# Kernel optimization log

Measured on AMD Instinct MI355X. Metric: run time of the kernel, lower is better.

The kernel has to match this reference:

```python
import jax, jax.numpy as jnp
import numpy as np

B, D, H, S = 65536, 256, 4, 64
HD = D // H  # head_dim = 64
EPS = 1e-8


def _lin(x, W, b):
    # torch nn.Linear: y = x @ W.T + b, W: [out, in]
    return x @ W.T + b


def _cos_attn(q_heads, keys, vals):
    # q_heads: [B,H,hd]; keys/vals: [H,S,hd] (shared across batch)
    qn = q_heads / (jnp.linalg.norm(q_heads, axis=-1, keepdims=True) + EPS)
    kn = keys / (jnp.linalg.norm(keys, axis=-1, keepdims=True) + EPS)
    sim = jnp.einsum('bhd,hsd->bhs', qn, kn)          # cosine sims, temp=1.0
    attn = jax.nn.softmax(sim, axis=-1)
    return jnp.einsum('bhs,hsd->bhd', attn, vals)     # [B,H,hd]


def setup_inputs() -> dict:
    key = jax.random.key(0)
    ks = jax.random.split(key, 20)

    def xavier(k, shape):
        fan_in, fan_out = shape[1], shape[0]
        lim = np.sqrt(6.0 / (fan_in + fan_out))
        return jax.random.uniform(k, shape, jnp.float32, -lim, lim)

    return {
        'query': jax.random.normal(ks[0], (B, D), jnp.float32),
        'context': jax.random.normal(ks[1], (B, D), jnp.float32),
        'fast_keys': 0.01 * jax.random.normal(ks[2], (H, S, HD), jnp.float32),
        'fast_vals': 0.01 * jax.random.normal(ks[3], (H, S, HD), jnp.float32),
        'deep_keys': 0.01 * jax.random.normal(ks[4], (H, S, HD), jnp.float32),
        'deep_vals': 0.01 * jax.random.normal(ks[5], (H, S, HD), jnp.float32),
        'Wq': xavier(ks[6], (D, D)), 'bq': jnp.zeros((D,), jnp.float32),
        'Wg': xavier(ks[7], (D, D)), 'bg': jnp.zeros((D,), jnp.float32),
        'Wc1': xavier(ks[8], (D // 2, D)), 'bc1': jnp.zeros((D // 2,), jnp.float32),
        'Wc2': xavier(ks[9], (1, D // 2)), 'bc2': jnp.zeros((1,), jnp.float32),
        'Wo': xavier(ks[10], (D, D)), 'bo': jnp.zeros((D,), jnp.float32),
        'Ws': xavier(ks[11], (D, D)), 'bs': jnp.zeros((D,), jnp.float32),
        'mix_logit': jnp.zeros((), jnp.float32),
        'surprise_mean': jnp.zeros((1, D), jnp.float32),
        'surprise_var': jnp.ones((1, D), jnp.float32),
    }


def reference(query, context, fast_keys, fast_vals, deep_keys, deep_vals,
              Wq, bq, Wg, bg, Wc1, bc1, Wc2, bc2, Wo, bo, Ws, bs,
              mix_logit, surprise_mean, surprise_var):
    # --- query projection and head split ---
    q = _lin(query, Wq, bq)                       # [B, D]
    q_heads = q.reshape(B, H, HD)                 # [B, H, hd]

    # --- dual-tier cosine-similarity attention reads ---
    v_fast = _cos_attn(q_heads, fast_keys, fast_vals).reshape(B, D)
    v_deep = _cos_attn(q_heads, deep_keys, deep_vals).reshape(B, D)

    # --- context-gated mixing of tiers ---
    gate = jnp.tanh(_lin(context, Wg, bg)).mean(axis=-1, keepdims=True)  # [B,1]
    mix = jax.nn.sigmoid(mix_logit + gate)
    out = mix * v_fast + (1.0 - mix) * v_deep

    # --- adaptive retrieval confidence head ---
    conf = jax.nn.sigmoid(_lin(jnp.tanh(_lin(context, Wc1, bc1)), Wc2, bc2))  # [B,1]
    out = out * conf
    out = _lin(out, Wo, bo)                       # [B, d_value]

    # --- surprise (detached diagnostic, does not feed output) ---
    h = jax.lax.stop_gradient(_lin(context, Ws, bs))
    z = (h - surprise_mean) / jnp.sqrt(surprise_var + 1e-6)
    surprise = jax.nn.sigmoid(jnp.abs(z).mean(axis=-1) - 2.0)  # 1/max(0.5,0.1)=2.0
    del surprise  # aux diagnostic; main output is the retrieved vector
    return out
```

## Files before the change

### kernel.cpp

```cpp
#include <hip/hip_runtime.h>

typedef unsigned short u16;
typedef __attribute__((ext_vector_type(8))) short bf16x8;
typedef __attribute__((ext_vector_type(4))) float f32x4;
typedef __attribute__((ext_vector_type(4))) unsigned short u16x4;

#define MFMA16(a, b, c) __builtin_amdgcn_mfma_f32_16x16x32_bf16((a), (b), (c), 0, 0, 0)

#define OFF_WQ   0
#define OFF_WG   65536
#define OFF_WC1  131072
#define OFF_WO   163840
#define OFF_KNF  229376
#define OFF_VTF  245760
#define OFF_KND  262144
#define OFF_VTD  278528

__device__ __forceinline__ u16 f2b(float f) {
  union { float f; unsigned u; } v; v.f = f;
  unsigned r = v.u + 0x7fffu + ((v.u >> 16) & 1u);
  return (u16)(r >> 16);
}
__device__ __forceinline__ float fsig(float x) {
  return __builtin_amdgcn_rcpf(1.f + __expf(-x));
}
__device__ __forceinline__ float ftanh(float x) {
  float e = __expf(2.f * x);
  return (e - 1.f) * __builtin_amdgcn_rcpf(e + 1.f);
}
__device__ __forceinline__ float sum16(float v) {
  v += __shfl_xor(v, 1);
  v += __shfl_xor(v, 2);
  v += __shfl_xor(v, 4);
  v += __shfl_xor(v, 8);
  return v;
}

__global__ void k_convert(const float* __restrict__ Wq, const float* __restrict__ Wg,
                          const float* __restrict__ Wc1, const float* __restrict__ Wo,
                          u16* __restrict__ ws) {
  int i = blockIdx.x * 256 + threadIdx.x;
  ws[OFF_WQ + i] = f2b(Wq[i]);
  ws[OFF_WG + i] = f2b(Wg[i]);
  ws[OFF_WO + i] = f2b(Wo[i]);
  if (i < 32768) ws[OFF_WC1 + i] = f2b(Wc1[i]);
}

__global__ void k_prep(const float* __restrict__ fk, const float* __restrict__ fv,
                       const float* __restrict__ dk, const float* __restrict__ dv,
                       u16* __restrict__ ws) {
  int t = blockIdx.x * 64 + threadIdx.x;
  int h = t >> 6, s = t & 63;
  const float* p;
  float ss, sc;

  p = fk + t * 64; ss = 0.f;
  for (int d = 0; d < 64; ++d) { float x = p[d]; ss += x * x; }
  sc = __builtin_amdgcn_rcpf(__builtin_amdgcn_sqrtf(ss) + 1e-8f);
  for (int d = 0; d < 64; ++d) ws[OFF_KNF + t * 64 + d] = f2b(p[d] * sc);

  p = dk + t * 64; ss = 0.f;
  for (int d = 0; d < 64; ++d) { float x = p[d]; ss += x * x; }
  sc = __builtin_amdgcn_rcpf(__builtin_amdgcn_sqrtf(ss) + 1e-8f);
  for (int d = 0; d < 64; ++d) ws[OFF_KND + t * 64 + d] = f2b(p[d] * sc);

  p = fv + t * 64;
  for (int d = 0; d < 64; ++d) ws[OFF_VTF + h * 4096 + d * 64 + s] = f2b(p[d]);
  p = dv + t * 64;
  for (int d = 0; d < 64; ++d) ws[OFF_VTD + h * 4096 + d * 64 + s] = f2b(p[d]);
}

__global__ __launch_bounds__(256, 2)
void k_fused(const float* __restrict__ query, const float* __restrict__ context,
             const float* __restrict__ bq, const float* __restrict__ bg,
             const float* __restrict__ bc1, const float* __restrict__ Wc2,
             const float* __restrict__ bc2v, const float* __restrict__ bo,
             const float* __restrict__ mixl, const u16* __restrict__ ws,
             float* __restrict__ outp) {
  __shared__ u16 sX[64 * 256];
  __shared__ float red_g[4][64];
  __shared__ float red_c[4][64];
  __shared__ float sA[64];
  __shared__ float sB[64];

  const int t = threadIdx.x;
  const int w = t >> 6;
  const int lane = t & 63;
  const int quad = lane >> 4;
  const int l16 = lane & 15;
  const int row4 = quad * 4;
  const int blk = blockIdx.x;
  char* Xb = (char*)sX;
  char* chunk = Xb + w * 8192;

  auto stage = [&](const float* src) {
    #pragma unroll
    for (int i = 0; i < 16; ++i) {
      int e = i * 1024 + t * 4;
      float4 v = *(const float4*)(src + e);
      int row = e >> 8, col = e & 255;
      u16x4 pk;
      pk.x = f2b(v.x); pk.y = f2b(v.y); pk.z = f2b(v.z); pk.w = f2b(v.w);
      *(u16x4*)(Xb + row * 512 + ((((col >> 3) ^ (row & 7)) << 4) | ((col & 7) << 1))) = pk;
    }
  };
  auto ldA = [&](int row, int kb) {
    return *(const bf16x8*)(Xb + row * 512 + ((((kb >> 3) ^ (row & 7)) << 4)));
  };
  auto ldC = [&](int row, int kb) {
    return *(const bf16x8*)(chunk + row * 128 + ((((kb >> 3) ^ (row & 7)) << 4)));
  };
  auto cwr = [&](int row, int col, u16 v) {
    *(u16*)(chunk + row * 128 + (((((col >> 3) ^ (row & 7)) << 3) | (col & 7)) << 1)) = v;
  };

  const f32x4 vzero = {0.f, 0.f, 0.f, 0.f};

  stage(context + (size_t)blk * 16384);
  __syncthreads();

  {
    f32x4 acc[4][4];
    #pragma unroll
    for (int mt = 0; mt < 4; ++mt)
      #pragma unroll
      for (int nt = 0; nt < 4; ++nt) acc[mt][nt] = vzero;
    const u16* WB = ws + OFF_WG + (w * 64 + l16) * 256;
    #pragma unroll
    for (int kk = 0; kk < 8; ++kk) {
      int kb = kk * 32 + quad * 8;
      bf16x8 a0 = ldA(l16, kb), a1 = ldA(16 + l16, kb), a2 = ldA(32 + l16, kb), a3 = ldA(48 + l16, kb);
      #pragma unroll
      for (int nt = 0; nt < 4; ++nt) {
        bf16x8 b = *(const bf16x8*)(WB + nt * 4096 + kb);
        acc[0][nt] = MFMA16(a0, b, acc[0][nt]);
        acc[1][nt] = MFMA16(a1, b, acc[1][nt]);
        acc[2][nt] = MFMA16(a2, b, acc[2][nt]);
        acc[3][nt] = MFMA16(a3, b, acc[3][nt]);
      }
    }
    float bgv[4];
    #pragma unroll
    for (int nt = 0; nt < 4; ++nt) bgv[nt] = bg[w * 64 + nt * 16 + l16];
    #pragma unroll
    for (int mt = 0; mt < 4; ++mt)
      #pragma unroll
      for (int r = 0; r < 4; ++r) {
        float s = 0.f;
        #pragma unroll
        for (int nt = 0; nt < 4; ++nt) s += ftanh(acc[mt][nt][r] + bgv[nt]);
        s = sum16(s);
        if (l16 == 0) red_g[w][mt * 16 + row4 + r] = s;
      }
  }
  {
    f32x4 acc[4][2];
    #pragma unroll
    for (int mt = 0; mt < 4; ++mt) { acc[mt][0] = vzero; acc[mt][1] = vzero; }
    const u16* WB = ws + OFF_WC1 + (w * 32 + l16) * 256;
    #pragma unroll
    for (int kk = 0; kk < 8; ++kk) {
      int kb = kk * 32 + quad * 8;
      bf16x8 a0 = ldA(l16, kb), a1 = ldA(16 + l16, kb), a2 = ldA(32 + l16, kb), a3 = ldA(48 + l16, kb);
      #pragma unroll
      for (int nt = 0; nt < 2; ++nt) {
        bf16x8 b = *(const bf16x8*)(WB + nt * 4096 + kb);
        acc[0][nt] = MFMA16(a0, b, acc[0][nt]);
        acc[1][nt] = MFMA16(a1, b, acc[1][nt]);
        acc[2][nt] = MFMA16(a2, b, acc[2][nt]);
        acc[3][nt] = MFMA16(a3, b, acc[3][nt]);
      }
    }
    float bcv[2], wcv[2];
    #pragma unroll
    for (int nt = 0; nt < 2; ++nt) {
      int n = w * 32 + nt * 16 + l16;
      bcv[nt] = bc1[n]; wcv[nt] = Wc2[n];
    }
    #pragma unroll
    for (int mt = 0; mt < 4; ++mt)
      #pragma unroll
      for (int r = 0; r < 4; ++r) {
        float s = 0.f;
        #pragma unroll
        for (int nt = 0; nt < 2; ++nt) s += ftanh(acc[mt][nt][r] + bcv[nt]) * wcv[nt];
        s = sum16(s);
        if (l16 == 0) red_c[w][mt * 16 + row4 + r] = s;
      }
  }
  __syncthreads();
  if (t < 64) {
    float g = (red_g[0][t] + red_g[1][t] + red_g[2][t] + red_g[3][t]) * (1.f / 256.f);
    float mix = fsig(mixl[0] + g);
    float conf = fsig(red_c[0][t] + red_c[1][t] + red_c[2][t] + red_c[3][t] + bc2v[0]);
    sA[t] = conf * mix;
    sB[t] = conf - conf * mix;
  }
  __syncthreads();

  stage(query + (size_t)blk * 16384);
  __syncthreads();

  f32x4 qa[4][4];
  {
    #pragma unroll
    for (int mt = 0; mt < 4; ++mt)
      #pragma unroll
      for (int nt = 0; nt < 4; ++nt) qa[mt][nt] = vzero;
    const u16* WB = ws + OFF_WQ + (w * 64 + l16) * 256;
    #pragma unroll
    for (int kk = 0; kk < 8; ++kk) {
      int kb = kk * 32 + quad * 8;
      bf16x8 a0 = ldA(l16, kb), a1 = ldA(16 + l16, kb), a2 = ldA(32 + l16, kb), a3 = ldA(48 + l16, kb);
      #pragma unroll
      for (int nt = 0; nt < 4; ++nt) {
        bf16x8 b = *(const bf16x8*)(WB + nt * 4096 + kb);
        qa[0][nt] = MFMA16(a0, b, qa[0][nt]);
        qa[1][nt] = MFMA16(a1, b, qa[1][nt]);
        qa[2][nt] = MFMA16(a2, b, qa[2][nt]);
        qa[3][nt] = MFMA16(a3, b, qa[3][nt]);
      }
    }
    float bqv[4];
    #pragma unroll
    for (int nt = 0; nt < 4; ++nt) bqv[nt] = bq[w * 64 + nt * 16 + l16];
    #pragma unroll
    for (int mt = 0; mt < 4; ++mt)
      #pragma unroll
      for (int nt = 0; nt < 4; ++nt)
        #pragma unroll
        for (int r = 0; r < 4; ++r) qa[mt][nt][r] += bqv[nt];
  }
  float scl[4][4];
  #pragma unroll
  for (int mt = 0; mt < 4; ++mt)
    #pragma unroll
    for (int r = 0; r < 4; ++r) {
      float ss = 0.f;
      #pragma unroll
      for (int nt = 0; nt < 4; ++nt) ss += qa[mt][nt][r] * qa[mt][nt][r];
      ss = sum16(ss);
      scl[mt][r] = __builtin_amdgcn_rcpf(__builtin_amdgcn_sqrtf(ss) + 1e-8f);
    }
  __syncthreads();

  #pragma unroll
  for (int mt = 0; mt < 4; ++mt)
    #pragma unroll
    for (int r = 0; r < 4; ++r) {
      int row = mt * 16 + row4 + r;
      #pragma unroll
      for (int nt = 0; nt < 4; ++nt)
        cwr(row, nt * 16 + l16, f2b(qa[mt][nt][r] * scl[mt][r]));
    }

  f32x4 sf[4][4], sd[4][4];
  #pragma unroll
  for (int mt = 0; mt < 4; ++mt)
    #pragma unroll
    for (int nt = 0; nt < 4; ++nt) { sf[mt][nt] = vzero; sd[mt][nt] = vzero; }
  {
    const u16* knF = ws + OFF_KNF + w * 4096;
    const u16* knD = ws + OFF_KND + w * 4096;
    #pragma unroll
    for (int kk = 0; kk < 2; ++kk) {
      int kb = kk * 32 + quad * 8;
      bf16x8 a0 = ldC(l16, kb), a1 = ldC(16 + l16, kb), a2 = ldC(32 + l16, kb), a3 = ldC(48 + l16, kb);
      #pragma unroll
      for (int nt = 0; nt < 4; ++nt) {
        bf16x8 bF = *(const bf16x8*)(knF + (nt * 16 + l16) * 64 + kb);
        bf16x8 bD = *(const bf16x8*)(knD + (nt * 16 + l16) * 64 + kb);
        sf[0][nt] = MFMA16(a0, bF, sf[0][nt]);
        sf[1][nt] = MFMA16(a1, bF, sf[1][nt]);
        sf[2][nt] = MFMA16(a2, bF, sf[2][nt]);
        sf[3][nt] = MFMA16(a3, bF, sf[3][nt]);
        sd[0][nt] = MFMA16(a0, bD, sd[0][nt]);
        sd[1][nt] = MFMA16(a1, bD, sd[1][nt]);
        sd[2][nt] = MFMA16(a2, bD, sd[2][nt]);
        sd[3][nt] = MFMA16(a3, bD, sd[3][nt]);
      }
    }
  }

  f32x4 oacc[4][4];
  {
    #pragma unroll
    for (int mt = 0; mt < 4; ++mt)
      #pragma unroll
      for (int r = 0; r < 4; ++r) {
        float rs = 0.f;
        #pragma unroll
        for (int nt = 0; nt < 4; ++nt) { float e = __expf(sf[mt][nt][r]); sf[mt][nt][r] = e; rs += e; }
        rs = sum16(rs);
        float inv = __builtin_amdgcn_rcpf(rs);
        int row = mt * 16 + row4 + r;
        #pragma unroll
        for (int nt = 0; nt < 4; ++nt) cwr(row, nt * 16 + l16, f2b(sf[mt][nt][r] * inv));
      }
    f32x4 pv[4][4];
    #pragma unroll
    for (int mt = 0; mt < 4; ++mt)
      #pragma unroll
      for (int nt = 0; nt < 4; ++nt) pv[mt][nt] = vzero;
    const u16* vT = ws + OFF_VTF + w * 4096;
    #pragma unroll
    for (int kk = 0; kk < 2; ++kk) {
      int kb = kk * 32 + quad * 8;
      bf16x8 a0 = ldC(l16, kb), a1 = ldC(16 + l16, kb), a2 = ldC(32 + l16, kb), a3 = ldC(48 + l16, kb);
      #pragma unroll
      for (int nt = 0; nt < 4; ++nt) {
        bf16x8 b = *(const bf16x8*)(vT + (nt * 16 + l16) * 64 + kb);
        pv[0][nt] = MFMA16(a0, b, pv[0][nt]);
        pv[1][nt] = MFMA16(a1, b, pv[1][nt]);
        pv[2][nt] = MFMA16(a2, b, pv[2][nt]);
        pv[3][nt] = MFMA16(a3, b, pv[3][nt]);
      }
    }
    #pragma unroll
    for (int mt = 0; mt < 4; ++mt)
      #pragma unroll
      for (int r = 0; r < 4; ++r) {
        float m_ = sA[mt * 16 + row4 + r];
        #pragma unroll
        for (int nt = 0; nt < 4; ++nt) oacc[mt][nt][r] = m_ * pv[mt][nt][r];
      }
  }
  {
    #pragma unroll
    for (int mt = 0; mt < 4; ++mt)
      #pragma unroll
      for (int r = 0; r < 4; ++r) {
        float rs = 0.f;
        #pragma unroll
        for (int nt = 0; nt < 4; ++nt) { float e = __expf(sd[mt][nt][r]); sd[mt][nt][r] = e; rs += e; }
        rs = sum16(rs);
        float inv = __builtin_amdgcn_rcpf(rs);
        int row = mt * 16 + row4 + r;
        #pragma unroll
        for (int nt = 0; nt < 4; ++nt) cwr(row, nt * 16 + l16, f2b(sd[mt][nt][r] * inv));
      }
    f32x4 pv[4][4];
    #pragma unroll
    for (int mt = 0; mt < 4; ++mt)
      #pragma unroll
      for (int nt = 0; nt < 4; ++nt) pv[mt][nt] = vzero;
    const u16* vT = ws + OFF_VTD + w * 4096;
    #pragma unroll
    for (int kk = 0; kk < 2; ++kk) {
      int kb = kk * 32 + quad * 8;
      bf16x8 a0 = ldC(l16, kb), a1 = ldC(16 + l16, kb), a2 = ldC(32 + l16, kb), a3 = ldC(48 + l16, kb);
      #pragma unroll
      for (int nt = 0; nt < 4; ++nt) {
        bf16x8 b = *(const bf16x8*)(vT + (nt * 16 + l16) * 64 + kb);
        pv[0][nt] = MFMA16(a0, b, pv[0][nt]);
        pv[1][nt] = MFMA16(a1, b, pv[1][nt]);
        pv[2][nt] = MFMA16(a2, b, pv[2][nt]);
        pv[3][nt] = MFMA16(a3, b, pv[3][nt]);
      }
    }
    #pragma unroll
    for (int mt = 0; mt < 4; ++mt)
      #pragma unroll
      for (int r = 0; r < 4; ++r) {
        float m_ = sB[mt * 16 + row4 + r];
        #pragma unroll
        for (int nt = 0; nt < 4; ++nt) oacc[mt][nt][r] += m_ * pv[mt][nt][r];
      }
  }

  __syncthreads();
  #pragma unroll
  for (int mt = 0; mt < 4; ++mt)
    #pragma unroll
    for (int r = 0; r < 4; ++r) {
      int row = mt * 16 + row4 + r;
      #pragma unroll
      for (int nt = 0; nt < 4; ++nt) {
        int col = w * 64 + nt * 16 + l16;
        *(u16*)(Xb + row * 512 + (((((col >> 3) ^ (row & 7)) << 3) | (col & 7)) << 1)) =
            f2b(oacc[mt][nt][r]);
      }
    }
  __syncthreads();

  {
    f32x4 o[4][4];
    #pragma unroll
    for (int mt = 0; mt < 4; ++mt)
      #pragma unroll
      for (int nt = 0; nt < 4; ++nt) o[mt][nt] = vzero;
    const u16* WB = ws + OFF_WO + (w * 64 + l16) * 256;
    #pragma unroll
    for (int kk = 0; kk < 8; ++kk) {
      int kb = kk * 32 + quad * 8;
      bf16x8 a0 = ldA(l16, kb), a1 = ldA(16 + l16, kb), a2 = ldA(32 + l16, kb), a3 = ldA(48 + l16, kb);
      #pragma unroll
      for (int nt = 0; nt < 4; ++nt) {
        bf16x8 b = *(const bf16x8*)(WB + nt * 4096 + kb);
        o[0][nt] = MFMA16(a0, b, o[0][nt]);
        o[1][nt] = MFMA16(a1, b, o[1][nt]);
        o[2][nt] = MFMA16(a2, b, o[2][nt]);
        o[3][nt] = MFMA16(a3, b, o[3][nt]);
      }
    }
    float bov[4];
    #pragma unroll
    for (int nt = 0; nt < 4; ++nt) bov[nt] = bo[w * 64 + nt * 16 + l16];
    float* dst = outp + (size_t)blk * 16384;
    #pragma unroll
    for (int mt = 0; mt < 4; ++mt)
      #pragma unroll
      for (int r = 0; r < 4; ++r) {
        int row = mt * 16 + row4 + r;
        #pragma unroll
        for (int nt = 0; nt < 4; ++nt)
          dst[row * 256 + w * 64 + nt * 16 + l16] = o[mt][nt][r] + bov[nt];
      }
  }
}

extern "C" void kernel_launch(void* const* d_in, const int* in_sizes, int n_in,
                              void* d_out, int out_size, void* d_ws, size_t ws_size,
                              hipStream_t stream) {
  const float* query   = (const float*)d_in[0];
  const float* context = (const float*)d_in[1];
  const float* fk      = (const float*)d_in[2];
  const float* fv      = (const float*)d_in[3];
  const float* dk      = (const float*)d_in[4];
  const float* dv      = (const float*)d_in[5];
  const float* Wq      = (const float*)d_in[6];
  const float* bq      = (const float*)d_in[7];
  const float* Wg      = (const float*)d_in[8];
  const float* bg      = (const float*)d_in[9];
  const float* Wc1     = (const float*)d_in[10];
  const float* bc1     = (const float*)d_in[11];
  const float* Wc2     = (const float*)d_in[12];
  const float* bc2     = (const float*)d_in[13];
  const float* Wo      = (const float*)d_in[14];
  const float* bo      = (const float*)d_in[15];
  const float* mixl    = (const float*)d_in[18];
  u16* ws = (u16*)d_ws;
  float* outp = (float*)d_out;

  k_convert<<<256, 256, 0, stream>>>(Wq, Wg, Wc1, Wo, ws);
  k_prep<<<4, 64, 0, stream>>>(fk, fv, dk, dv, ws);
  k_fused<<<1024, 256, 0, stream>>>(query, context, bq, bg, bc1, Wc2, bc2, bo,
                                    mixl, ws, outp);
}
```

Baseline: 323.9 us.

## Halve rows per block to raise occupancy and parallelize key prep per element

The fused kernel now processes 32 batch rows per block instead of 64, using twice as many blocks, half the shared memory and half the accumulator registers, with launch bounds raised to 4 blocks per CU. The key/value prep kernel is reworked from one thread per key row with serial loops into one block per key row, with a wave-wide shuffle reduction for the norm. This aims to improve latency hiding and remove the serial prep bottleneck. In exchange, each weight B-fragment loaded from global memory is reused across only two M-tiles instead of four, so weight traffic per row doubles.

```diff
diff --git a/kernel.cpp b/kernel.cpp
--- a/kernel.cpp
+++ b/kernel.cpp
@@ -35,6 +35,15 @@
   v += __shfl_xor(v, 8);
   return v;
 }
+__device__ __forceinline__ float sum64(float v) {
+  v += __shfl_xor(v, 1);
+  v += __shfl_xor(v, 2);
+  v += __shfl_xor(v, 4);
+  v += __shfl_xor(v, 8);
+  v += __shfl_xor(v, 16);
+  v += __shfl_xor(v, 32);
+  return v;
+}
 
 __global__ void k_convert(const float* __restrict__ Wq, const float* __restrict__ Wg,
                           const float* __restrict__ Wc1, const float* __restrict__ Wo,
@@ -49,39 +58,36 @@
 __global__ void k_prep(const float* __restrict__ fk, const float* __restrict__ fv,
                        const float* __restrict__ dk, const float* __restrict__ dv,
                        u16* __restrict__ ws) {
-  int t = blockIdx.x * 64 + threadIdx.x;
+  int t = blockIdx.x;
   int h = t >> 6, s = t & 63;
-  const float* p;
-  float ss, sc;
-
-  p = fk + t * 64; ss = 0.f;
-  for (int d = 0; d < 64; ++d) { float x = p[d]; ss += x * x; }
+  int d = threadIdx.x;
+
+  float x = fk[t * 64 + d];
+  float ss = sum64(x * x);
+  float sc = __builtin_amdgcn_rcpf(__builtin_amdgcn_sqrtf(ss) + 1e-8f);
+  ws[OFF_KNF + t * 64 + d] = f2b(x * sc);
+
+  x = dk[t * 64 + d];
+  ss = sum64(x * x);
   sc = __builtin_amdgcn_rcpf(__builtin_amdgcn_sqrtf(ss) + 1e-8f);
-  for (int d = 0; d < 64; ++d) ws[OFF_KNF + t * 64 + d] = f2b(p[d] * sc);
-
-  p = dk + t * 64; ss = 0.f;
-  for (int d = 0; d < 64; ++d) { float x = p[d]; ss += x * x; }
-  sc = __builtin_amdgcn_rcpf(__builtin_amdgcn_sqrtf(ss) + 1e-8f);
-  for (int d = 0; d < 64; ++d) ws[OFF_KND + t * 64 + d] = f2b(p[d] * sc);
-
-  p = fv + t * 64;
-  for (int d = 0; d < 64; ++d) ws[OFF_VTF + h * 4096 + d * 64 + s] = f2b(p[d]);
-  p = dv + t * 64;
-  for (int d = 0; d < 64; ++d) ws[OFF_VTD + h * 4096 + d * 64 + s] = f2b(p[d]);
-}
-
-__global__ __launch_bounds__(256, 2)
+  ws[OFF_KND + t * 64 + d] = f2b(x * sc);
+
+  ws[OFF_VTF + h * 4096 + d * 64 + s] = f2b(fv[t * 64 + d]);
+  ws[OFF_VTD + h * 4096 + d * 64 + s] = f2b(dv[t * 64 + d]);
+}
+
+__global__ __launch_bounds__(256, 4)
 void k_fused(const float* __restrict__ query, const float* __restrict__ context,
              const float* __restrict__ bq, const float* __restrict__ bg,
              const float* __restrict__ bc1, const float* __restrict__ Wc2,
              const float* __restrict__ bc2v, const float* __restrict__ bo,
              const float* __restrict__ mixl, const u16* __restrict__ ws,
              float* __restrict__ outp) {
-  __shared__ u16 sX[64 * 256];
-  __shared__ float red_g[4][64];
-  __shared__ float red_c[4][64];
-  __shared__ float sA[64];
-  __shared__ float sB[64];
+  __shared__ u16 sX[32 * 256];
+  __shared__ float red_g[4][32];
+  __shared__ float red_c[4][32];
+  __shared__ float sA[32];
+  __shared__ float sB[32];
 
   const int t = threadIdx.x;
   const int w = t >> 6;
@@ -91,11 +97,11 @@
   const int row4 = quad * 4;
   const int blk = blockIdx.x;
   char* Xb = (char*)sX;
-  char* chunk = Xb + w * 8192;
+  char* chunk = Xb + w * 4096;
 
   auto stage = [&](const float* src) {
     #pragma unroll
-    for (int i = 0; i < 16; ++i) {
+    for (int i = 0; i < 8; ++i) {
       int e = i * 1024 + t * 4;
       float4 v = *(const float4*)(src + e);
       int row = e >> 8, col = e & 255;
@@ -116,34 +122,32 @@
 
   const f32x4 vzero = {0.f, 0.f, 0.f, 0.f};
 
-  stage(context + (size_t)blk * 16384);
-  __syncthreads();
-
-  {
-    f32x4 acc[4][4];
-    #pragma unroll
-    for (int mt = 0; mt < 4; ++mt)
+  stage(context + (size_t)blk * 8192);
+  __syncthreads();
+
+  {
+    f32x4 acc[2][4];
+    #pragma unroll
+    for (int mt = 0; mt < 2; ++mt)
       #pragma unroll
       for (int nt = 0; nt < 4; ++nt) acc[mt][nt] = vzero;
     const u16* WB = ws + OFF_WG + (w * 64 + l16) * 256;
     #pragma unroll
     for (int kk = 0; kk < 8; ++kk) {
       int kb = kk * 32 + quad * 8;
-      bf16x8 a0 = ldA(l16, kb), a1 = ldA(16 + l16, kb), a2 = ldA(32 + l16, kb), a3 = ldA(48 + l16, kb);
+      bf16x8 a0 = ldA(l16, kb), a1 = ldA(16 + l16, kb);
       #pragma unroll
       for (int nt = 0; nt < 4; ++nt) {
         bf16x8 b = *(const bf16x8*)(WB + nt * 4096 + kb);
         acc[0][nt] = MFMA16(a0, b, acc[0][nt]);
         acc[1][nt] = MFMA16(a1, b, acc[1][nt]);
-        acc[2][nt] = MFMA16(a2, b, acc[2][nt]);
-        acc[3][nt] = MFMA16(a3, b, acc[3][nt]);
       }
     }
     float bgv[4];
     #pragma unroll
     for (int nt = 0; nt < 4; ++nt) bgv[nt] = bg[w * 64 + nt * 16 + l16];
     #pragma unroll
-    for (int mt = 0; mt < 4; ++mt)
+    for (int mt = 0; mt < 2; ++mt)
       #pragma unroll
       for (int r = 0; r < 4; ++r) {
         float s = 0.f;
@@ -154,21 +158,19 @@
       }
   }
   {
-    f32x4 acc[4][2];
-    #pragma unroll
-    for (int mt = 0; mt < 4; ++mt) { acc[mt][0] = vzero; acc[mt][1] = vzero; }
+    f32x4 acc[2][2];
+    #pragma unroll
+    for (int mt = 0; mt < 2; ++mt) { acc[mt][0] = vzero; acc[mt][1] = vzero; }
     const u16* WB = ws + OFF_WC1 + (w * 32 + l16) * 256;
     #pragma unroll
     for (int kk = 0; kk < 8; ++kk) {
       int kb = kk * 32 + quad * 8;
-      bf16x8 a0 = ldA(l16, kb), a1 = ldA(16 + l16, kb), a2 = ldA(32 + l16, kb), a3 = ldA(48 + l16, kb);
+      bf16x8 a0 = ldA(l16, kb), a1 = ldA(16 + l16, kb);
       #pragma unroll
       for (int nt = 0; nt < 2; ++nt) {
         bf16x8 b = *(const bf16x8*)(WB + nt * 4096 + kb);
         acc[0][nt] = MFMA16(a0, b, acc[0][nt]);
         acc[1][nt] = MFMA16(a1, b, acc[1][nt]);
-        acc[2][nt] = MFMA16(a2, b, acc[2][nt]);
-        acc[3][nt] = MFMA16(a3, b, acc[3][nt]);
       }
     }
     float bcv[2], wcv[2];
@@ -178,7 +180,7 @@
       bcv[nt] = bc1[n]; wcv[nt] = Wc2[n];
     }
     #pragma unroll
-    for (int mt = 0; mt < 4; ++mt)
+    for (int mt = 0; mt < 2; ++mt)
       #pragma unroll
       for (int r = 0; r < 4; ++r) {
         float s = 0.f;
@@ -189,7 +191,7 @@
       }
   }
   __syncthreads();
-  if (t < 64) {
+  if (t < 32) {
     float g = (red_g[0][t] + red_g[1][t] + red_g[2][t] + red_g[3][t]) * (1.f / 256.f);
     float mix = fsig(mixl[0] + g);
     float conf = fsig(red_c[0][t] + red_c[1][t] + red_c[2][t] + red_c[3][t] + bc2v[0]);
@@ -198,42 +200,40 @@
   }
   __syncthreads();
 
-  stage(query + (size_t)blk * 16384);
-  __syncthreads();
-
-  f32x4 qa[4][4];
-  {
-    #pragma unroll
-    for (int mt = 0; mt < 4; ++mt)
+  stage(query + (size_t)blk * 8192);
+  __syncthreads();
+
+  f32x4 qa[2][4];
+  {
+    #pragma unroll
+    for (int mt = 0; mt < 2; ++mt)
       #pragma unroll
       for (int nt = 0; nt < 4; ++nt) qa[mt][nt] = vzero;
     const u16* WB = ws + OFF_WQ + (w * 64 + l16) * 256;
     #pragma unroll
     for (int kk = 0; kk < 8; ++kk) {
       int kb = kk * 32 + quad * 8;
-      bf16x8 a0 = ldA(l16, kb), a1 = ldA(16 + l16, kb), a2 = ldA(32 + l16, kb), a3 = ldA(48 + l16, kb);
+      bf16x8 a0 = ldA(l16, kb), a1 = ldA(16 + l16, kb);
       #pragma unroll
       for (int nt = 0; nt < 4; ++nt) {
         bf16x8 b = *(const bf16x8*)(WB + nt * 4096 + kb);
         qa[0][nt] = MFMA16(a0, b, qa[0][nt]);
         qa[1][nt] = MFMA16(a1, b, qa[1][nt]);
-        qa[2][nt] = MFMA16(a2, b, qa[2][nt]);
-        qa[3][nt] = MFMA16(a3, b, qa[3][nt]);
       }
     }
     float bqv[4];
     #pragma unroll
     for (int nt = 0; nt < 4; ++nt) bqv[nt] = bq[w * 64 + nt * 16 + l16];
     #pragma unroll
-    for (int mt = 0; mt < 4; ++mt)
+    for (int mt = 0; mt < 2; ++mt)
       #pragma unroll
       for (int nt = 0; nt < 4; ++nt)
         #pragma unroll
         for (int r = 0; r < 4; ++r) qa[mt][nt][r] += bqv[nt];
   }
-  float scl[4][4];
+  float scl[2][4];
   #pragma unroll
-  for (int mt = 0; mt < 4; ++mt)
+  for (int mt = 0; mt < 2; ++mt)
     #pragma unroll
     for (int r = 0; r < 4; ++r) {
       float ss = 0.f;
@@ -245,7 +245,7 @@
   __syncthreads();
 
   #pragma unroll
-  for (int mt = 0; mt < 4; ++mt)
+  for (int mt = 0; mt < 2; ++mt)
     #pragma unroll
     for (int r = 0; r < 4; ++r) {
       int row = mt * 16 + row4 + r;
@@ -254,9 +254,9 @@
         cwr(row, nt * 16 + l16, f2b(qa[mt][nt][r] * scl[mt][r]));
     }
 
-  f32x4 sf[4][4], sd[4][4];
+  f32x4 sf[2][4], sd[2][4];
   #pragma unroll
-  for (int mt = 0; mt < 4; ++mt)
+  for (int mt = 0; mt < 2; ++mt)
     #pragma unroll
     for (int nt = 0; nt < 4; ++nt) { sf[mt][nt] = vzero; sd[mt][nt] = vzero; }
   {
@@ -265,27 +265,23 @@
     #pragma unroll
     for (int kk = 0; kk < 2; ++kk) {
       int kb = kk * 32 + quad * 8;
-      bf16x8 a0 = ldC(l16, kb), a1 = ldC(16 + l16, kb), a2 = ldC(32 + l16, kb), a3 = ldC(48 + l16, kb);
+      bf16x8 a0 = ldC(l16, kb), a1 = ldC(16 + l16, kb);
       #pragma unroll
       for (int nt = 0; nt < 4; ++nt) {
         bf16x8 bF = *(const bf16x8*)(knF + (nt * 16 + l16) * 64 + kb);
         bf16x8 bD = *(const bf16x8*)(knD + (nt * 16 + l16) * 64 + kb);
         sf[0][nt] = MFMA16(a0, bF, sf[0][nt]);
         sf[1][nt] = MFMA16(a1, bF, sf[1][nt]);
-        sf[2][nt] = MFMA16(a2, bF, sf[2][nt]);
-        sf[3][nt] = MFMA16(a3, bF, sf[3][nt]);
         sd[0][nt] = MFMA16(a0, bD, sd[0][nt]);
         sd[1][nt] = MFMA16(a1, bD, sd[1][nt]);
-        sd[2][nt] = MFMA16(a2, bD, sd[2][nt]);
-        sd[3][nt] = MFMA16(a3, bD, sd[3][nt]);
-      }
-    }
-  }
-
-  f32x4 oacc[4][4];
-  {
-    #pragma unroll
-    for (int mt = 0; mt < 4; ++mt)
+      }
+    }
+  }
+
+  f32x4 oacc[2][4];
+  {
+    #pragma unroll
+    for (int mt = 0; mt < 2; ++mt)
       #pragma unroll
       for (int r = 0; r < 4; ++r) {
         float rs = 0.f;
@@ -297,27 +293,25 @@
         #pragma unroll
         for (int nt = 0; nt < 4; ++nt) cwr(row, nt * 16 + l16, f2b(sf[mt][nt][r] * inv));
       }
-    f32x4 pv[4][4];
-    #pragma unroll
-    for (int mt = 0; mt < 4; ++mt)
+    f32x4 pv[2][4];
+    #pragma unroll
+    for (int mt = 0; mt < 2; ++mt)
       #pragma unroll
       for (int nt = 0; nt < 4; ++nt) pv[mt][nt] = vzero;
     const u16* vT = ws + OFF_VTF + w * 4096;
     #pragma unroll
     for (int kk = 0; kk < 2; ++kk) {
       int kb = kk * 32 + quad * 8;
-      bf16x8 a0 = ldC(l16, kb), a1 = ldC(16 + l16, kb), a2 = ldC(32 + l16, kb), a3 = ldC(48 + l16, kb);
+      bf16x8 a0 = ldC(l16, kb), a1 = ldC(16 + l16, kb);
       #pragma unroll
       for (int nt = 0; nt < 4; ++nt) {
         bf16x8 b = *(const bf16x8*)(vT + (nt * 16 + l16) * 64 + kb);
         pv[0][nt] = MFMA16(a0, b, pv[0][nt]);
         pv[1][nt] = MFMA16(a1, b, pv[1][nt]);
-        pv[2][nt] = MFMA16(a2, b, pv[2][nt]);
-        pv[3][nt] = MFMA16(a3, b, pv[3][nt]);
-      }
-    }
-    #pragma unroll
-    for (int mt = 0; mt < 4; ++mt)
+      }
+    }
+    #pragma unroll
+    for (int mt = 0; mt < 2; ++mt)
       #pragma unroll
       for (int r = 0; r < 4; ++r) {
         float m_ = sA[mt * 16 + row4 + r];
@@ -327,7 +321,7 @@
   }
   {
     #pragma unroll
-    for (int mt = 0; mt < 4; ++mt)
+    for (int mt = 0; mt < 2; ++mt)
       #pragma unroll
       for (int r = 0; r < 4; ++r) {
         float rs = 0.f;
@@ -339,27 +333,25 @@
         #pragma unroll
         for (int nt = 0; nt < 4; ++nt) cwr(row, nt * 16 + l16, f2b(sd[mt][nt][r] * inv));
       }
-    f32x4 pv[4][4];
-    #pragma unroll
-    for (int mt = 0; mt < 4; ++mt)
+    f32x4 pv[2][4];
+    #pragma unroll
+    for (int mt = 0; mt < 2; ++mt)
       #pragma unroll
       for (int nt = 0; nt < 4; ++nt) pv[mt][nt] = vzero;
     const u16* vT = ws + OFF_VTD + w * 4096;
     #pragma unroll
     for (int kk = 0; kk < 2; ++kk) {
       int kb = kk * 32 + quad * 8;
-      bf16x8 a0 = ldC(l16, kb), a1 = ldC(16 + l16, kb), a2 = ldC(32 + l16, kb), a3 = ldC(48 + l16, kb);
+      bf16x8 a0 = ldC(l16, kb), a1 = ldC(16 + l16, kb);
       #pragma unroll
       for (int nt = 0; nt < 4; ++nt) {
         bf16x8 b = *(const bf16x8*)(vT + (nt * 16 + l16) * 64 + kb);
         pv[0][nt] = MFMA16(a0, b, pv[0][nt]);
         pv[1][nt] = MFMA16(a1, b, pv[1][nt]);
-        pv[2][nt] = MFMA16(a2, b, pv[2][nt]);
-        pv[3][nt] = MFMA16(a3, b, pv[3][nt]);
-      }
-    }
-    #pragma unroll
-    for (int mt = 0; mt < 4; ++mt)
+      }
+    }
+    #pragma unroll
+    for (int mt = 0; mt < 2; ++mt)
       #pragma unroll
       for (int r = 0; r < 4; ++r) {
         float m_ = sB[mt * 16 + row4 + r];
@@ -370,7 +362,7 @@
 
   __syncthreads();
   #pragma unroll
-  for (int mt = 0; mt < 4; ++mt)
+  for (int mt = 0; mt < 2; ++mt)
     #pragma unroll
     for (int r = 0; r < 4; ++r) {
       int row = mt * 16 + row4 + r;
@@ -384,31 +376,29 @@
   __syncthreads();
 
   {
-    f32x4 o[4][4];
-    #pragma unroll
-    for (int mt = 0; mt < 4; ++mt)
+    f32x4 o[2][4];
+    #pragma unroll
+    for (int mt = 0; mt < 2; ++mt)
       #pragma unroll
       for (int nt = 0; nt < 4; ++nt) o[mt][nt] = vzero;
     const u16* WB = ws + OFF_WO + (w * 64 + l16) * 256;
     #pragma unroll
     for (int kk = 0; kk < 8; ++kk) {
       int kb = kk * 32 + quad * 8;
-      bf16x8 a0 = ldA(l16, kb), a1 = ldA(16 + l16, kb), a2 = ldA(32 + l16, kb), a3 = ldA(48 + l16, kb);
+      bf16x8 a0 = ldA(l16, kb), a1 = ldA(16 + l16, kb);
       #pragma unroll
       for (int nt = 0; nt < 4; ++nt) {
         bf16x8 b = *(const bf16x8*)(WB + nt * 4096 + kb);
         o[0][nt] = MFMA16(a0, b, o[0][nt]);
         o[1][nt] = MFMA16(a1, b, o[1][nt]);
-        o[2][nt] = MFMA16(a2, b, o[2][nt]);
-        o[3][nt] = MFMA16(a3, b, o[3][nt]);
       }
     }
     float bov[4];
     #pragma unroll
     for (int nt = 0; nt < 4; ++nt) bov[nt] = bo[w * 64 + nt * 16 + l16];
-    float* dst = outp + (size_t)blk * 16384;
-    #pragma unroll
-    for (int mt = 0; mt < 4; ++mt)
+    float* dst = outp + (size_t)blk * 8192;
+    #pragma unroll
+    for (int mt = 0; mt < 2; ++mt)
       #pragma unroll
       for (int r = 0; r < 4; ++r) {
         int row = mt * 16 + row4 + r;
@@ -443,7 +433,7 @@
   float* outp = (float*)d_out;
 
   k_convert<<<256, 256, 0, stream>>>(Wq, Wg, Wc1, Wo, ws);
-  k_prep<<<4, 64, 0, stream>>>(fk, fv, dk, dv, ws);
-  k_fused<<<1024, 256, 0, stream>>>(query, context, bq, bg, bc1, Wc2, bc2, bo,
+  k_prep<<<256, 64, 0, stream>>>(fk, fv, dk, dv, ws);
+  k_fused<<<2048, 256, 0, stream>>>(query, context, bq, bg, bc1, Wc2, bc2, bo,
                                     mixl, ws, outp);
 }
```

Result: slower. 331.7 us (+2.4%).
